# Kernel tuning notes

Hardware: AMD Instinct MI355X
Metric: run time of the kernel (lower is better)

The kernel has to match this reference:

```python
import jax, jax.numpy as jnp
import numpy as np

B, S, H, E, K = 4, 4096, 2048, 64, 8
SEQ_ALPHA = 0.01


def setup_inputs() -> dict:
    key = jax.random.key(0)
    k1, k2 = jax.random.split(key)
    x = jax.random.normal(k1, (B, S, H), dtype=jnp.float32)
    # kaiming_uniform_(a=sqrt(5)) on [E, H] -> bound = 1/sqrt(H)
    bound = 1.0 / np.sqrt(H)
    weight = jax.random.uniform(k2, (E, H), dtype=jnp.float32, minval=-bound, maxval=bound)
    expert_bias = jnp.zeros((E,), dtype=jnp.float32)
    return {"x": x, "weight": weight, "expert_bias": expert_bias}


def reference(x, weight, expert_bias):
    bsz, seq_len, _ = x.shape
    x_flat = x.reshape(-1, x.shape[-1])                      # [T, H], T = B*S
    logits = x_flat @ weight.T                               # [T, E]
    scores = jax.nn.sigmoid(logits)
    biased_logits = logits + expert_bias[None, :]
    _, topk_idx = jax.lax.top_k(biased_logits, K)            # [T, K] int32
    topk_w = jnp.take_along_axis(scores, topk_idx, axis=-1)  # [T, K]
    topk_w = topk_w / (topk_w.sum(axis=-1, keepdims=True) + 1e-10)  # K > 1
    # load stats (training-mode bincount)
    expert_load = jnp.bincount(topk_idx.reshape(-1), length=E).astype(jnp.int64)
    # sequence-wise balance loss (DeepSeek-V3)
    scores_r = scores.reshape(bsz, seq_len, E)
    expert_mask = jax.nn.one_hot(topk_idx.reshape(bsz, -1), E, dtype=scores.dtype)  # [B, S*K, E]
    f_i = expert_mask.sum(axis=1) / (K * seq_len)            # [B, E]
    normalized = scores_r / (scores_r.sum(axis=2, keepdims=True) + 1e-10)
    P_i = normalized.mean(axis=1)                            # [B, E]
    aux_seq_loss = SEQ_ALPHA * (f_i * P_i).sum(axis=1).mean()
    return (topk_idx, topk_w, aux_seq_loss, expert_load)
```

## Files before the change

kernel.cpp:

```cpp
#include <hip/hip_runtime.h>
#include <math.h>

#define HDIM 2048
#define TTOK 16384
#define NEXP 64
#define TOPK 8
#define SLEN 4096
#define NBATCH 4
#define PARTSZ (NEXP * TTOK)

#define OFF_W    131072
#define OFF_LOSS 262144
#define OFF_LOAD 262145

#define WS_PACC 0
#define WS_CACC 256
#define WS_CNT  512
#define WS_WT   1024
#define WS_PART (1024 + HDIM * NEXP)

__global__ __launch_bounds__(256) void transpose_w(const float* __restrict__ W,
                                                   float* __restrict__ Wt) {
  __shared__ float tile[64][65];
  const int tid = threadIdx.x;
  const int k0 = blockIdx.x * 64;
  {
    const int kc = (tid & 15) << 2;
    const int er = tid >> 4;
#pragma unroll
    for (int i = 0; i < 4; ++i) {
      int e = er + i * 16;
      float4 v = *(const float4*)(W + (size_t)e * HDIM + k0 + kc);
      tile[e][kc + 0] = v.x; tile[e][kc + 1] = v.y;
      tile[e][kc + 2] = v.z; tile[e][kc + 3] = v.w;
    }
  }
  __syncthreads();
  {
    const int e4 = (tid & 15) << 2;
    const int kr = tid >> 4;
#pragma unroll
    for (int i = 0; i < 4; ++i) {
      int k = kr + i * 16;
      float4 v;
      v.x = tile[e4 + 0][k]; v.y = tile[e4 + 1][k];
      v.z = tile[e4 + 2][k]; v.w = tile[e4 + 3][k];
      *(float4*)(Wt + (size_t)(k0 + k) * NEXP + e4) = v;
    }
  }
}

template <int KS>
__global__ __launch_bounds__(512, 8) void gate_gemm(
    const float* __restrict__ x,
    const float* __restrict__ Wt,
    float* __restrict__ part) {
  constexpr int KR = HDIM / KS;
  constexpr int NT = KR / 32;
  __shared__ float xs[2][128 * 32];

  const int tid = threadIdx.x;
  const int lane = tid & 63;
  const int wv = __builtin_amdgcn_readfirstlane(tid >> 6);
  const int eg = wv & 3;
  const int th = wv >> 2;
  const int bid = blockIdx.x;
  const int kh = bid & (KS - 1);
  const int tg = bid >> (KS == 8 ? 3 : 2);
  const int tok0 = tg << 7;
  const int kb = kh * KR;

  float acc[16];
#pragma unroll
  for (int j = 0; j < 16; ++j) acc[j] = 0.f;

  const int r0 = tid >> 3;
  const int sg = tid & 7;
  const int sslot = (sg ^ (r0 & 7)) << 2;
  const float* xp0 = x + (size_t)(tok0 + r0) * HDIM + kb + (sg << 2);
  const float* xp1 = xp0 + (size_t)64 * HDIM;
  float4 a0 = *(const float4*)xp0;
  float4 a1 = *(const float4*)xp1;

  const int myrow = (th << 6) + lane;
  const int rbase = myrow << 5;
  const int rs = lane & 7;

  for (int kt = 0; kt < NT; ++kt) {
    float* xb = &xs[kt & 1][0];
    *(float4*)&xb[(r0 << 5) + sslot] = a0;
    *(float4*)&xb[((r0 + 64) << 5) + sslot] = a1;
    __syncthreads();
    if (kt + 1 < NT) {
      a0 = *(const float4*)(xp0 + ((kt + 1) << 5));
      a1 = *(const float4*)(xp1 + ((kt + 1) << 5));
    }
    const float* wkb = Wt + ((size_t)(kb + (kt << 5)) << 6) + (eg << 4);
#pragma unroll
    for (int c = 0; c < 8; ++c) {
      float4 xv = *(const float4*)&xb[rbase + ((c ^ rs) << 2)];
      const float xf[4] = {xv.x, xv.y, xv.z, xv.w};
#pragma unroll
      for (int q = 0; q < 4; ++q) {
        const float* wr = wkb + (((c << 2) + q) << 6);
#pragma unroll
        for (int j = 0; j < 16; ++j) acc[j] = fmaf(xf[q], wr[j], acc[j]);
      }
    }
  }

  float* dst = part + (size_t)kh * PARTSZ + ((size_t)(eg << 4)) * TTOK + tok0 +
               (th << 6) + lane;
#pragma unroll
  for (int j = 0; j < 16; ++j) dst[(size_t)j * TTOK] = acc[j];
}

template <int KS>
__global__ __launch_bounds__(128) void gate_epilogue(
    const float* __restrict__ part, const float* __restrict__ bias,
    float* __restrict__ out, float* __restrict__ Pacc,
    float* __restrict__ Cacc, int* __restrict__ counter) {
  __shared__ float le[64][65];
  __shared__ float rinv_sh[64];
  __shared__ unsigned csum[64];
  __shared__ int lastf;

  const int tid = threadIdx.x;
  const int t0 = blockIdx.x << 6;

  if (tid < 64) csum[tid] = 0u;

#pragma unroll
  for (int w = 0; w < 8; ++w) {
    const int f = (w << 7) + tid;
    const int e = f >> 4;
    const int q = f & 15;
    const float* p = part + (size_t)e * TTOK + t0 + (q << 2);
    float4 v[KS];
#pragma unroll
    for (int s = 0; s < KS; ++s) v[s] = *(const float4*)(p + (size_t)s * PARTSZ);
    float4 r;
    if (KS == 8) {
      r.x = ((v[0].x + v[1].x) + (v[2].x + v[3].x)) + ((v[4].x + v[5].x) + (v[6].x + v[7].x));
      r.y = ((v[0].y + v[1].y) + (v[2].y + v[3].y)) + ((v[4].y + v[5].y) + (v[6].y + v[7].y));
      r.z = ((v[0].z + v[1].z) + (v[2].z + v[3].z)) + ((v[4].z + v[5].z) + (v[6].z + v[7].z));
      r.w = ((v[0].w + v[1].w) + (v[2].w + v[3].w)) + ((v[4].w + v[5].w) + (v[6].w + v[7].w));
    } else {
      r.x = (v[0].x + v[1].x) + (v[2].x + v[3].x);
      r.y = (v[0].y + v[1].y) + (v[2].y + v[3].y);
      r.z = (v[0].z + v[1].z) + (v[2].z + v[3].z);
      r.w = (v[0].w + v[1].w) + (v[2].w + v[3].w);
    }
    le[e][(q << 2) + 0] = r.x; le[e][(q << 2) + 1] = r.y;
    le[e][(q << 2) + 2] = r.z; le[e][(q << 2) + 3] = r.w;
  }
  __syncthreads();

  if (tid < 64) {
    float bl[64];
    float ssum = 0.f;
#pragma unroll
    for (int e = 0; e < NEXP; ++e) {
      float l = le[e][tid];
      ssum += 1.f / (1.f + expf(-l));
      bl[e] = l + bias[e];
    }
    rinv_sh[tid] = 1.f / (ssum + 1e-10f);

    unsigned long long chosen = 0ull;
    int i8[TOPK];
    float w8[TOPK];
    float wsum = 0.f;
#pragma unroll
    for (int j = 0; j < TOPK; ++j) {
      float best = -1e30f;
      int bi = 0;
      float braw = 0.f;
#pragma unroll
      for (int e = 0; e < NEXP; ++e) {
        bool ok = (((chosen >> e) & 1ull) == 0ull) && (bl[e] > best);
        if (ok) { best = bl[e]; bi = e; braw = bl[e] - bias[e]; }
      }
      chosen |= (1ull << bi);
      float sc = 1.f / (1.f + expf(-braw));
      i8[j] = bi;
      w8[j] = sc;
      wsum += sc;
    }
    const float inv = 1.f / (wsum + 1e-10f);
    const int t = t0 + tid;
    float4 o;
    o.x = (float)i8[0]; o.y = (float)i8[1]; o.z = (float)i8[2]; o.w = (float)i8[3];
    *(float4*)(out + (size_t)t * TOPK) = o;
    o.x = (float)i8[4]; o.y = (float)i8[5]; o.z = (float)i8[6]; o.w = (float)i8[7];
    *(float4*)(out + (size_t)t * TOPK + 4) = o;
    o.x = w8[0] * inv; o.y = w8[1] * inv; o.z = w8[2] * inv; o.w = w8[3] * inv;
    *(float4*)(out + OFF_W + (size_t)t * TOPK) = o;
    o.x = w8[4] * inv; o.y = w8[5] * inv; o.z = w8[6] * inv; o.w = w8[7] * inv;
    *(float4*)(out + OFF_W + (size_t)t * TOPK + 4) = o;
#pragma unroll
    for (int j = 0; j < TOPK; ++j) atomicAdd(&csum[i8[j]], 1u);
  }
  __syncthreads();

  const int b = blockIdx.x >> 6;
  if (tid < 64) {
    float p = 0.f;
    for (int tt = 0; tt < 64; ++tt) {
      float sc = 1.f / (1.f + expf(-le[tid][tt]));
      p += sc * rinv_sh[tt];
    }
    atomicAdd(&Pacc[(b << 6) + tid], p);
    atomicAdd(&Cacc[(b << 6) + tid], (float)csum[tid]);
  }
  __syncthreads();
  __threadfence();
  if (tid == 0) {
    int old = __hip_atomic_fetch_add(counter, 1, __ATOMIC_ACQ_REL,
                                     __HIP_MEMORY_SCOPE_AGENT);
    lastf = (old == 255) ? 1 : 0;
  }
  __syncthreads();

  if (lastf && tid < 64) {
    const int e = tid;
    float load = 0.f, partl = 0.f;
#pragma unroll
    for (int bb = 0; bb < NBATCH; ++bb) {
      float c = __hip_atomic_load(&Cacc[(bb << 6) + e], __ATOMIC_RELAXED,
                                  __HIP_MEMORY_SCOPE_AGENT);
      float p = __hip_atomic_load(&Pacc[(bb << 6) + e], __ATOMIC_RELAXED,
                                  __HIP_MEMORY_SCOPE_AGENT);
      load += c;
      partl += (c * (1.f / (TOPK * (float)SLEN))) * (p * (1.f / (float)SLEN));
    }
    out[OFF_LOAD + e] = load;
#pragma unroll
    for (int off = 32; off; off >>= 1) partl += __shfl_down(partl, off);
    if (e == 0) out[OFF_LOSS] = 0.01f * partl * (1.f / (float)NBATCH);
  }
}

extern "C" void kernel_launch(void* const* d_in, const int* in_sizes, int n_in,
                              void* d_out, int out_size, void* d_ws, size_t ws_size,
                              hipStream_t stream) {
  const float* x = (const float*)d_in[0];
  const float* W = (const float*)d_in[1];
  const float* bias = (const float*)d_in[2];
  float* out = (float*)d_out;

  float* ws = (float*)d_ws;
  float* Pacc = ws + WS_PACC;
  float* Cacc = ws + WS_CACC;
  int* counter = (int*)(ws + WS_CNT);
  float* Wt = ws + WS_WT;
  float* part = ws + WS_PART;

  hipMemsetAsync(ws, 0, WS_WT * sizeof(float), stream);
  transpose_w<<<32, 256, 0, stream>>>(W, Wt);

  const size_t need8 = ((size_t)WS_PART + 8 * (size_t)PARTSZ) * sizeof(float);
  if (ws_size >= need8) {
    gate_gemm<8><<<1024, 512, 0, stream>>>(x, Wt, part);
    gate_epilogue<8><<<256, 128, 0, stream>>>(part, bias, out, Pacc, Cacc, counter);
  } else {
    gate_gemm<4><<<512, 512, 0, stream>>>(x, Wt, part);
    gate_epilogue<4><<<256, 128, 0, stream>>>(part, bias, out, Pacc, Cacc, counter);
  }
}
```

Measured before the change: 268.9 us.

## Double per-thread token tile in gate GEMM and widen epilogue to 128 tokens

The gate GEMM now runs 256-thread blocks where each wave covers 16 experts for all 128 tokens. Each thread accumulates two token rows, so every weight load feeds two FMAs instead of one, which cuts weight-load traffic per FMA. The epilogue handles 128 tokens per block with all 128 threads doing top-k, and it splits the P-sum across both halves of the block. The fallback for a small workspace with KS=4 is removed, so the code assumes the workspace can hold 8 partial slices. Register pressure rises with 32 accumulators per thread, and the epilogue grid now has only 128 blocks.

```diff
diff --git a/kernel.cpp b/kernel.cpp
--- a/kernel.cpp
+++ b/kernel.cpp
@@ -7,6 +7,8 @@
 #define TOPK 8
 #define SLEN 4096
 #define NBATCH 4
+#define KS 8
+#define KR 256
 #define PARTSZ (NEXP * TTOK)
 
 #define OFF_W    131072
@@ -50,118 +52,122 @@
   }
 }
 
-template <int KS>
-__global__ __launch_bounds__(512, 8) void gate_gemm(
+__global__ __launch_bounds__(256, 4) void gate_gemm(
     const float* __restrict__ x,
     const float* __restrict__ Wt,
     float* __restrict__ part) {
-  constexpr int KR = HDIM / KS;
-  constexpr int NT = KR / 32;
   __shared__ float xs[2][128 * 32];
 
   const int tid = threadIdx.x;
   const int lane = tid & 63;
   const int wv = __builtin_amdgcn_readfirstlane(tid >> 6);
-  const int eg = wv & 3;
-  const int th = wv >> 2;
+  const int e0 = wv << 4;
   const int bid = blockIdx.x;
-  const int kh = bid & (KS - 1);
-  const int tg = bid >> (KS == 8 ? 3 : 2);
+  const int kh = bid & 7;
+  const int tg = bid >> 3;
   const int tok0 = tg << 7;
-  const int kb = kh * KR;
-
-  float acc[16];
-#pragma unroll
-  for (int j = 0; j < 16; ++j) acc[j] = 0.f;
-
-  const int r0 = tid >> 3;
-  const int sg = tid & 7;
-  const int sslot = (sg ^ (r0 & 7)) << 2;
-  const float* xp0 = x + (size_t)(tok0 + r0) * HDIM + kb + (sg << 2);
-  const float* xp1 = xp0 + (size_t)64 * HDIM;
-  float4 a0 = *(const float4*)xp0;
-  float4 a1 = *(const float4*)xp1;
-
-  const int myrow = (th << 6) + lane;
-  const int rbase = myrow << 5;
-  const int rs = lane & 7;
-
-  for (int kt = 0; kt < NT; ++kt) {
+  const int kb = kh << 8;
+
+  float acc0[16], acc1[16];
+#pragma unroll
+  for (int j = 0; j < 16; ++j) { acc0[j] = 0.f; acc1[j] = 0.f; }
+
+  const int sr = tid >> 1;
+  const int sh = tid & 1;
+  const float* xp = x + (size_t)(tok0 + sr) * HDIM + kb + (sh << 4);
+  float4 a[4];
+#pragma unroll
+  for (int i = 0; i < 4; ++i) a[i] = *(const float4*)(xp + (i << 2));
+
+  const int s0 = lane & 7;
+  const int r0 = lane << 5;
+  const int r1 = (lane + 64) << 5;
+  const int sbase = sr << 5;
+  const int s7 = sr & 7;
+
+  for (int kt = 0; kt < 8; ++kt) {
     float* xb = &xs[kt & 1][0];
-    *(float4*)&xb[(r0 << 5) + sslot] = a0;
-    *(float4*)&xb[((r0 + 64) << 5) + sslot] = a1;
+#pragma unroll
+    for (int i = 0; i < 4; ++i) {
+      const int g = (sh << 2) + i;
+      *(float4*)&xb[sbase + ((g ^ s7) << 2)] = a[i];
+    }
     __syncthreads();
-    if (kt + 1 < NT) {
-      a0 = *(const float4*)(xp0 + ((kt + 1) << 5));
-      a1 = *(const float4*)(xp1 + ((kt + 1) << 5));
-    }
-    const float* wkb = Wt + ((size_t)(kb + (kt << 5)) << 6) + (eg << 4);
+    if (kt < 7) {
+      const float* np_ = xp + ((kt + 1) << 5);
+#pragma unroll
+      for (int i = 0; i < 4; ++i) a[i] = *(const float4*)(np_ + (i << 2));
+    }
+    const float* wkb = Wt + ((size_t)(kb + (kt << 5)) << 6) + e0;
 #pragma unroll
     for (int c = 0; c < 8; ++c) {
-      float4 xv = *(const float4*)&xb[rbase + ((c ^ rs) << 2)];
-      const float xf[4] = {xv.x, xv.y, xv.z, xv.w};
+      float4 xv0 = *(const float4*)&xb[r0 + ((c ^ s0) << 2)];
+      float4 xv1 = *(const float4*)&xb[r1 + ((c ^ s0) << 2)];
+      const float xf0[4] = {xv0.x, xv0.y, xv0.z, xv0.w};
+      const float xf1[4] = {xv1.x, xv1.y, xv1.z, xv1.w};
 #pragma unroll
       for (int q = 0; q < 4; ++q) {
         const float* wr = wkb + (((c << 2) + q) << 6);
-#pragma unroll
-        for (int j = 0; j < 16; ++j) acc[j] = fmaf(xf[q], wr[j], acc[j]);
+        const float xa = xf0[q];
+        const float xc = xf1[q];
+#pragma unroll
+        for (int j = 0; j < 16; ++j) {
+          acc0[j] = fmaf(xa, wr[j], acc0[j]);
+          acc1[j] = fmaf(xc, wr[j], acc1[j]);
+        }
       }
     }
   }
 
-  float* dst = part + (size_t)kh * PARTSZ + ((size_t)(eg << 4)) * TTOK + tok0 +
-               (th << 6) + lane;
-#pragma unroll
-  for (int j = 0; j < 16; ++j) dst[(size_t)j * TTOK] = acc[j];
-}
-
-template <int KS>
+  float* dst = part + (size_t)kh * PARTSZ + (size_t)e0 * TTOK + tok0 + lane;
+#pragma unroll
+  for (int j = 0; j < 16; ++j) {
+    dst[(size_t)j * TTOK] = acc0[j];
+    dst[(size_t)j * TTOK + 64] = acc1[j];
+  }
+}
+
 __global__ __launch_bounds__(128) void gate_epilogue(
     const float* __restrict__ part, const float* __restrict__ bias,
     float* __restrict__ out, float* __restrict__ Pacc,
     float* __restrict__ Cacc, int* __restrict__ counter) {
-  __shared__ float le[64][65];
-  __shared__ float rinv_sh[64];
+  __shared__ float le[128 * 65];
+  __shared__ float rinv_sh[128];
+  __shared__ float psum[64];
   __shared__ unsigned csum[64];
   __shared__ int lastf;
 
   const int tid = threadIdx.x;
-  const int t0 = blockIdx.x << 6;
-
-  if (tid < 64) csum[tid] = 0u;
-
-#pragma unroll
-  for (int w = 0; w < 8; ++w) {
-    const int f = (w << 7) + tid;
-    const int e = f >> 4;
-    const int q = f & 15;
+  const int t0 = blockIdx.x << 7;
+
+  if (tid < 64) { psum[tid] = 0.f; csum[tid] = 0u; }
+
+#pragma unroll
+  for (int i = 0; i < 16; ++i) {
+    const int idx = (i << 7) + tid;
+    const int e = idx >> 5;
+    const int q = idx & 31;
     const float* p = part + (size_t)e * TTOK + t0 + (q << 2);
     float4 v[KS];
 #pragma unroll
     for (int s = 0; s < KS; ++s) v[s] = *(const float4*)(p + (size_t)s * PARTSZ);
-    float4 r;
-    if (KS == 8) {
-      r.x = ((v[0].x + v[1].x) + (v[2].x + v[3].x)) + ((v[4].x + v[5].x) + (v[6].x + v[7].x));
-      r.y = ((v[0].y + v[1].y) + (v[2].y + v[3].y)) + ((v[4].y + v[5].y) + (v[6].y + v[7].y));
-      r.z = ((v[0].z + v[1].z) + (v[2].z + v[3].z)) + ((v[4].z + v[5].z) + (v[6].z + v[7].z));
-      r.w = ((v[0].w + v[1].w) + (v[2].w + v[3].w)) + ((v[4].w + v[5].w) + (v[6].w + v[7].w));
-    } else {
-      r.x = (v[0].x + v[1].x) + (v[2].x + v[3].x);
-      r.y = (v[0].y + v[1].y) + (v[2].y + v[3].y);
-      r.z = (v[0].z + v[1].z) + (v[2].z + v[3].z);
-      r.w = (v[0].w + v[1].w) + (v[2].w + v[3].w);
-    }
-    le[e][(q << 2) + 0] = r.x; le[e][(q << 2) + 1] = r.y;
-    le[e][(q << 2) + 2] = r.z; le[e][(q << 2) + 3] = r.w;
-  }
-  __syncthreads();
-
-  if (tid < 64) {
+    float r[4];
+    const float* f = (const float*)v;
+#pragma unroll
+    for (int j = 0; j < 4; ++j)
+      r[j] = ((f[j] + f[4 + j]) + (f[8 + j] + f[12 + j])) +
+             ((f[16 + j] + f[20 + j]) + (f[24 + j] + f[28 + j]));
+#pragma unroll
+    for (int j = 0; j < 4; ++j) le[((q << 2) + j) * 65 + e] = r[j];
+  }
+  __syncthreads();
+
+  {
     float bl[64];
     float ssum = 0.f;
 #pragma unroll
     for (int e = 0; e < NEXP; ++e) {
-      float l = le[e][tid];
+      float l = le[tid * 65 + e];
       ssum += 1.f / (1.f + expf(-l));
       bl[e] = l + bias[e];
     }
@@ -203,14 +209,23 @@
   }
   __syncthreads();
 
-  const int b = blockIdx.x >> 6;
+  {
+    const int e = tid & 63;
+    const int ch = tid >> 6;
+    float p = 0.f;
+#pragma unroll 8
+    for (int tt = 0; tt < 64; ++tt) {
+      const int tok = (ch << 6) + tt;
+      float sc = 1.f / (1.f + expf(-le[tok * 65 + e]));
+      p += sc * rinv_sh[tok];
+    }
+    atomicAdd(&psum[e], p);
+  }
+  __syncthreads();
+
+  const int b = blockIdx.x >> 5;
   if (tid < 64) {
-    float p = 0.f;
-    for (int tt = 0; tt < 64; ++tt) {
-      float sc = 1.f / (1.f + expf(-le[tid][tt]));
-      p += sc * rinv_sh[tt];
-    }
-    atomicAdd(&Pacc[(b << 6) + tid], p);
+    atomicAdd(&Pacc[(b << 6) + tid], psum[tid]);
     atomicAdd(&Cacc[(b << 6) + tid], (float)csum[tid]);
   }
   __syncthreads();
@@ -218,7 +233,7 @@
   if (tid == 0) {
     int old = __hip_atomic_fetch_add(counter, 1, __ATOMIC_ACQ_REL,
                                      __HIP_MEMORY_SCOPE_AGENT);
-    lastf = (old == 255) ? 1 : 0;
+    lastf = (old == 127) ? 1 : 0;
   }
   __syncthreads();
 
@@ -258,13 +273,6 @@
 
   hipMemsetAsync(ws, 0, WS_WT * sizeof(float), stream);
   transpose_w<<<32, 256, 0, stream>>>(W, Wt);
-
-  const size_t need8 = ((size_t)WS_PART + 8 * (size_t)PARTSZ) * sizeof(float);
-  if (ws_size >= need8) {
-    gate_gemm<8><<<1024, 512, 0, stream>>>(x, Wt, part);
-    gate_epilogue<8><<<256, 128, 0, stream>>>(part, bias, out, Pacc, Cacc, counter);
-  } else {
-    gate_gemm<4><<<512, 512, 0, stream>>>(x, Wt, part);
-    gate_epilogue<4><<<256, 128, 0, stream>>>(part, bias, out, Pacc, Cacc, counter);
-  }
-}
+  gate_gemm<<<1024, 256, 0, stream>>>(x, Wt, part);
+  gate_epilogue<<<128, 128, 0, stream>>>(part, bias, out, Pacc, Cacc, counter);
+}
```

Measured after the change: 275.4 us. 1.02x slower.
